# Performance work log

Measured on AMD Instinct MI355X. Metric: run time of the kernel, lower is better.

Reference implementation:

```python
import jax, jax.numpy as jnp
import numpy as np

B, T, D, H = 2, 2048, 1024, 16
DK = D // H
SCALE = 1.0 / float(np.sqrt(DK))


def setup_inputs() -> dict:
    key0 = jax.random.key(0)
    ks = jax.random.split(key0, 12)
    std = 0.02
    inp = {
        "query": jax.random.normal(ks[0], (B, T, D), jnp.float32),
        "key": jax.random.normal(ks[1], (B, T, D), jnp.float32),
        "value": jax.random.normal(ks[2], (B, T, D), jnp.float32),
        # weights stored torch-style: out = x @ W.T + b, W is [D, D]
        "Wq": jax.random.normal(ks[3], (D, D), jnp.float32) * std,
        "bq": jnp.zeros((D,), jnp.float32),
        "Wk": jax.random.normal(ks[4], (D, D), jnp.float32) * std,
        "bk": jnp.zeros((D,), jnp.float32),
        "Wv": jax.random.normal(ks[5], (D, D), jnp.float32) * std,
        "bv": jnp.zeros((D,), jnp.float32),
        "Wo": jax.random.normal(ks[6], (D, D), jnp.float32) * std,
        "bo": jnp.zeros((D,), jnp.float32),
        # causal mask: True = masked out (matches masked_fill semantics)
        "attn_mask": jnp.triu(jnp.ones((T, T), jnp.bool_), k=1),
        # no padding (all False) to keep every softmax row valid
        "key_padding_mask": jnp.zeros((B, T), jnp.bool_),
    }
    return inp


def reference(query, key, value, Wq, bq, Wk, bk, Wv, bv, Wo, bo,
              attn_mask, key_padding_mask):
    Bq, Tq, _ = query.shape
    Tk = key.shape[1]
    # QKV projections, split into heads: [B, T, H, DK]
    q = (query @ Wq.T + bq).reshape(Bq, Tq, H, DK)
    k = (key @ Wk.T + bk).reshape(Bq, Tk, H, DK)
    v = (value @ Wv.T + bv).reshape(Bq, Tk, H, DK)
    # scaled dot-product scores: [B, H, Tq, Tk]
    scores = jnp.einsum("bqhd,bkhd->bhqk", q, k) * jnp.float32(SCALE)
    neg_inf = jnp.float32(-jnp.inf)
    scores = jnp.where(attn_mask[None, None, :, :], neg_inf, scores)
    scores = jnp.where(key_padding_mask[:, None, None, :], neg_inf, scores)
    attn = jax.nn.softmax(scores, axis=-1)
    out = jnp.einsum("bhqk,bkhd->bqhd", attn, v).reshape(Bq, Tq, D)
    return out @ Wo.T + bo
```

## Files before the change

kernel.cpp:

```cpp
#include <hip/hip_runtime.h>
#include <hip/hip_bf16.h>
#include <stdint.h>

#define B_   2
#define T_   2048
#define D_   1024
#define H_   16
#define DK_  64
#define KL2_ 0.18033688f

typedef __attribute__((ext_vector_type(8))) short   short8;
typedef __attribute__((ext_vector_type(4))) float   floatx4;
typedef unsigned short ushort_t;
typedef unsigned int   uint_t;

__device__ __forceinline__ ushort_t f32_to_bf16(float f) {
    union { float f; unsigned int u; } v; v.f = f;
    unsigned int r = v.u + 0x7fffu + ((v.u >> 16) & 1u);
    return (ushort_t)(r >> 16);
}

__device__ __forceinline__ uint_t pk_bf16(float lo, float hi) {
    uint_t ulo = __builtin_bit_cast(uint_t, lo) + 0x8000u;
    uint_t uhi = __builtin_bit_cast(uint_t, hi) + 0x8000u;
    return __builtin_amdgcn_perm(uhi, ulo, 0x07060302);
}

__device__ __forceinline__ void async_copy16(const ushort_t* g, ushort_t* l) {
    typedef const unsigned int __attribute__((address_space(1)))* gp_t;
    typedef       unsigned int __attribute__((address_space(3)))* lp_t;
    __builtin_amdgcn_global_load_lds((gp_t)(uintptr_t)g, (lp_t)(uintptr_t)l, 16, 0, 0);
}

__global__ __launch_bounds__(256) void cast_all_kernel(
    const float* __restrict__ q, const float* __restrict__ k, const float* __restrict__ v,
    const float* __restrict__ wq, const float* __restrict__ wk,
    const float* __restrict__ wv, const float* __restrict__ wo,
    ushort_t* __restrict__ oq, ushort_t* __restrict__ ok, ushort_t* __restrict__ ov,
    ushort_t* __restrict__ owq, ushort_t* __restrict__ owk,
    ushort_t* __restrict__ owv, ushort_t* __restrict__ owo)
{
    const int NTD4 = (B_ * T_ * D_) / 4;
    const int NW4  = (D_ * D_) / 4;
    int i = blockIdx.x * 256 + threadIdx.x;
    const float* s; ushort_t* d; int off;
    if (i < NTD4)              { s = q; d = oq; off = i; }
    else if (i < 2 * NTD4)     { s = k; d = ok; off = i - NTD4; }
    else if (i < 3 * NTD4)     { s = v; d = ov; off = i - 2 * NTD4; }
    else {
        int w = i - 3 * NTD4;
        int seg = w / NW4;  off = w - seg * NW4;
        s = (seg == 0) ? wq : (seg == 1) ? wk : (seg == 2) ? wv : wo;
        d = (seg == 0) ? owq : (seg == 1) ? owk : (seg == 2) ? owv : owo;
    }
    float4 x = ((const float4*)s)[off];
    ushort4 o;
    o.x = f32_to_bf16(x.x); o.y = f32_to_bf16(x.y);
    o.z = f32_to_bf16(x.z); o.w = f32_to_bf16(x.w);
    ((ushort4*)d)[off] = o;
}

#define BM 128
#define BK 32

template<int MODE, int NI>
__device__ __forceinline__ void gemm_bt_device(
    const ushort_t* __restrict__ A, const ushort_t* __restrict__ W,
    const float* __restrict__ bias, void* __restrict__ outp,
    int m0, int n0, ushort_t* sm, float oscale)
{
    const int tid  = threadIdx.x;
    const int lane = tid & 63;
    const int wv   = tid >> 6;
    const int wm   = (wv >> 1) * 64;
    const int wn   = (wv & 1) * (NI * 16);
    const int cl   = lane & 15;
    const int qd   = lane >> 4;
    const int sw4  = (cl >> 1) & 3;

    floatx4 acc[4][NI];
    const floatx4 z4 = {0.f, 0.f, 0.f, 0.f};
    #pragma unroll
    for (int mi = 0; mi < 4; ++mi)
        #pragma unroll
        for (int ni = 0; ni < NI; ++ni) acc[mi][ni] = z4;

    const int r0 = tid >> 2;
    const int cg = (tid & 3) ^ ((r0 >> 1) & 3);
    const ushort_t* Ag0 = A + (size_t)(m0 + r0) * 1024 + cg * 8;
    const ushort_t* Ag1 = A + (size_t)(m0 + 64 + r0) * 1024 + cg * 8;
    const ushort_t* Wg0 = W + (size_t)(n0 + r0) * 1024 + cg * 8;
    const ushort_t* Wg1 = W + (size_t)(n0 + 64 + r0) * 1024 + cg * 8;
    ushort_t* As0 = sm + tid * 8;
    ushort_t* As1 = sm + 2048 + tid * 8;
    ushort_t* Bs0 = sm + 4096 + tid * 8;
    ushort_t* Bs1 = sm + 6144 + tid * 8;

    for (int k0 = 0; k0 < 1024; k0 += BK) {
        async_copy16(Ag0 + k0, As0);
        async_copy16(Ag1 + k0, As1);
        async_copy16(Wg0 + k0, Bs0);
        if (NI == 4) async_copy16(Wg1 + k0, Bs1);
        __syncthreads();

        short8 af[4], bfr[NI];
        #pragma unroll
        for (int mi = 0; mi < 4; ++mi)
            af[mi] = *(const short8*)(sm + (wm + mi * 16 + cl) * 32 + (qd ^ sw4) * 8);
        #pragma unroll
        for (int ni = 0; ni < NI; ++ni)
            bfr[ni] = *(const short8*)(sm + 4096 + (wn + ni * 16 + cl) * 32 + (qd ^ sw4) * 8);

        #pragma unroll
        for (int mi = 0; mi < 4; ++mi)
            #pragma unroll
            for (int ni = 0; ni < NI; ++ni)
                acc[mi][ni] = __builtin_amdgcn_mfma_f32_16x16x32_bf16(
                    af[mi], bfr[ni], acc[mi][ni], 0, 0, 0);
        __syncthreads();
    }

    #pragma unroll
    for (int mi = 0; mi < 4; ++mi) {
        #pragma unroll
        for (int ni = 0; ni < NI; ++ni) {
            const int n = n0 + wn + ni * 16 + cl;
            const float bn = bias[n];
            if (MODE == 0) {
                float* out = (float*)outp;
                #pragma unroll
                for (int r = 0; r < 4; ++r) {
                    const int m = m0 + wm + mi * 16 + qd * 4 + r;
                    out[(size_t)m * D_ + n] = acc[mi][ni][r] + bn;
                }
            } else if (MODE == 1) {
                ushort_t* out = (ushort_t*)outp;
                const int h = n >> 6, dk = n & 63;
                #pragma unroll
                for (int r = 0; r < 4; ++r) {
                    const int m = m0 + wm + mi * 16 + qd * 4 + r;
                    const int b = m >> 11, t = m & (T_ - 1);
                    out[(((size_t)(b * H_ + h)) * T_ + t) * DK_ + dk] =
                        f32_to_bf16((acc[mi][ni][r] + bn) * oscale);
                }
            } else {
                ushort_t* out = (ushort_t*)outp;
                const int h = n >> 6, dk = n & 63;
                const int mb = m0 + wm + mi * 16 + qd * 4;
                const int b = mb >> 11, t0 = mb & (T_ - 1);
                const int tsw = (t0 & ~60) | ((t0 & 48) >> 2) | ((t0 & 12) << 2);
                ushort4 o;
                o.x = f32_to_bf16(acc[mi][ni][0] + bn);
                o.y = f32_to_bf16(acc[mi][ni][1] + bn);
                o.z = f32_to_bf16(acc[mi][ni][2] + bn);
                o.w = f32_to_bf16(acc[mi][ni][3] + bn);
                *(ushort4*)(out + (((size_t)(b * H_ + h)) * DK_ + dk) * T_ + tsw) = o;
            }
        }
    }
}

__global__ __launch_bounds__(256) void gemm_qkv_kernel(
    const ushort_t* __restrict__ Xq, const ushort_t* __restrict__ Xk, const ushort_t* __restrict__ Xv,
    const ushort_t* __restrict__ Wq, const ushort_t* __restrict__ Wk, const ushort_t* __restrict__ Wv,
    const float* __restrict__ bq, const float* __restrict__ bk, const float* __restrict__ bv,
    ushort_t* __restrict__ Q, ushort_t* __restrict__ K, ushort_t* __restrict__ Vt)
{
    __shared__ __align__(16) ushort_t sm[8192];
    const int m0 = blockIdx.x * BM, n0 = blockIdx.y * 128;
    if (blockIdx.z == 0)      gemm_bt_device<1, 4>(Xq, Wq, bq, Q,  m0, n0, sm, KL2_);
    else if (blockIdx.z == 1) gemm_bt_device<1, 4>(Xk, Wk, bk, K,  m0, n0, sm, 1.0f);
    else                      gemm_bt_device<2, 4>(Xv, Wv, bv, Vt, m0, n0, sm, 1.0f);
}

__global__ __launch_bounds__(256) void gemm_o_kernel(
    const ushort_t* __restrict__ A, const ushort_t* __restrict__ W,
    const float* __restrict__ bias, float* __restrict__ out)
{
    __shared__ __align__(16) ushort_t sm[8192];
    gemm_bt_device<0, 2>(A, W, bias, out, blockIdx.x * BM, blockIdx.y * 64, sm, 1.0f);
}

__global__ __launch_bounds__(256, 2) void attn_kernel(
    const ushort_t* __restrict__ Q, const ushort_t* __restrict__ K,
    const ushort_t* __restrict__ Vs, ushort_t* __restrict__ O)
{
    __shared__ __align__(16) ushort_t sm[32768];
    const int tid  = threadIdx.x;
    const int lane = tid & 63;
    const int wv   = tid >> 6;
    const int cl   = lane & 15;
    const int qd   = lane >> 4;
    const int swz  = cl & 7;
    const int h = blockIdx.x & (H_ - 1), b = blockIdx.x >> 4;
    const int p   = blockIdx.y;
    const int btA = 31 - p;

    const ushort_t* Qh = Q  + ((size_t)(b * H_ + h) * T_) * DK_;
    const ushort_t* Kh = K  + ((size_t)(b * H_ + h) * T_) * DK_;
    const ushort_t* Vh = Vs + ((size_t)(b * H_ + h) * DK_) * T_;

    const int sr  = tid >> 3;
    const int sc  = tid & 7;
    const int scg = sc ^ (sr & 7);

    auto stage_step = [&](int s) {
        const int kbase = ((s <= btA) ? s : (s - btA - 1)) << 6;
        ushort_t* Kb = sm + (s & 3) * 8192;
        ushort_t* Vb = Kb + 4096;
        #pragma unroll
        for (int rr = 0; rr < 2; ++rr) {
            const int r = rr * 32 + sr;
            async_copy16(Kh + (size_t)(kbase + r) * DK_ + scg * 8, Kb + r * 64 + sc * 8);
            async_copy16(Vh + (size_t)r * T_ + kbase + scg * 8,    Vb + r * 64 + sc * 8);
        }
    };

    int qw = btA * 64 + wv * 16;
    short8 qf0 = *(const short8*)(Qh + (size_t)(qw + cl) * DK_ + qd * 8);
    short8 qf1 = *(const short8*)(Qh + (size_t)(qw + cl) * DK_ + 32 + qd * 8);

    stage_step(0);
    stage_step(1);

    const floatx4 z4 = {0.f, 0.f, 0.f, 0.f};
    floatx4 oaccT[4] = {z4, z4, z4, z4};
    float l_ = 0.f;

    auto flush = [&](int q0w) {
        float l = l_;
        l += __shfl_xor(l, 16, 64);
        l += __shfl_xor(l, 32, 64);
        const float inv = 1.0f / l;
        ushort_t* Ob = O + ((size_t)(b * T_ + q0w + cl)) * D_ + h * DK_ + qd * 4;
        #pragma unroll
        for (int dt = 0; dt < 4; ++dt) {
            ushort4 o;
            o.x = f32_to_bf16(oaccT[dt][0] * inv);
            o.y = f32_to_bf16(oaccT[dt][1] * inv);
            o.z = f32_to_bf16(oaccT[dt][2] * inv);
            o.w = f32_to_bf16(oaccT[dt][3] * inv);
            *(ushort4*)(Ob + dt * 16) = o;
        }
    };

    auto compute_step = [&](int s) {
        const bool inA  = (s <= btA);
        const int kbase = (inA ? s : (s - btA - 1)) << 6;
        const bool diag = inA ? (s == btA) : (s == 32);
        ushort_t* cb = sm + (s & 3) * 8192;
        short8 kb[4][2];
        #pragma unroll
        for (int m = 0; m < 4; ++m)
            #pragma unroll
            for (int i = 0; i < 2; ++i)
                kb[m][i] = *(const short8*)(cb + (m * 16 + cl) * 64 + ((i * 4 + qd) ^ swz) * 8);
        floatx4 sacc[4] = {z4, z4, z4, z4};
        #pragma unroll
        for (int i = 0; i < 2; ++i)
            #pragma unroll
            for (int m = 0; m < 4; ++m)
                sacc[m] = __builtin_amdgcn_mfma_f32_16x16x32_bf16(
                    kb[m][i], (i ? qf1 : qf0), sacc[m], 0, 0, 0);
        const int qabs = qw + cl;
        float pr[4][4];
        if (diag) {
            #pragma unroll
            for (int c = 0; c < 4; ++c)
                #pragma unroll
                for (int r = 0; r < 4; ++r) {
                    const bool keep = (kbase + c * 16 + qd * 4 + r) <= qabs;
                    const float e = __builtin_amdgcn_exp2f(sacc[c][r]);
                    pr[c][r] = keep ? e : 0.f;
                    l_ += pr[c][r];
                }
        } else {
            #pragma unroll
            for (int c = 0; c < 4; ++c)
                #pragma unroll
                for (int r = 0; r < 4; ++r) {
                    pr[c][r] = __builtin_amdgcn_exp2f(sacc[c][r]);
                    l_ += pr[c][r];
                }
        }
        short8 va2[4][2];
        #pragma unroll
        for (int dt = 0; dt < 4; ++dt)
            #pragma unroll
            for (int h2 = 0; h2 < 2; ++h2)
                va2[dt][h2] = *(const short8*)(cb + 4096 + (dt * 16 + cl) * 64 +
                                               ((qd * 2 + h2) ^ swz) * 8);
        #pragma unroll
        for (int cp = 0; cp < 2; ++cp) {
            union { uint_t u[4]; short8 v; } pb;
            pb.u[0] = pk_bf16(pr[cp * 2][0],     pr[cp * 2][1]);
            pb.u[1] = pk_bf16(pr[cp * 2][2],     pr[cp * 2][3]);
            pb.u[2] = pk_bf16(pr[cp * 2 + 1][0], pr[cp * 2 + 1][1]);
            pb.u[3] = pk_bf16(pr[cp * 2 + 1][2], pr[cp * 2 + 1][3]);
            #pragma unroll
            for (int dt = 0; dt < 4; ++dt)
                oaccT[dt] = __builtin_amdgcn_mfma_f32_16x16x32_bf16(
                    va2[dt][cp], pb.v, oaccT[dt], 0, 0, 0);
        }
        if (s == btA) {
            flush(qw);
            #pragma unroll
            for (int dt = 0; dt < 4; ++dt) oaccT[dt] = z4;
            l_ = 0.f;
            qw = p * 64 + wv * 16;
            qf0 = *(const short8*)(Qh + (size_t)(qw + cl) * DK_ + qd * 8);
            qf1 = *(const short8*)(Qh + (size_t)(qw + cl) * DK_ + 32 + qd * 8);
        }
    };

    for (int g = 0; g < 17; ++g) {
        const int s0 = g * 2;
        __syncthreads();
        if (s0 + 2 <= 32) stage_step(s0 + 2);
        if (s0 + 3 <= 32) stage_step(s0 + 3);
        compute_step(s0);
        if (s0 + 1 <= 32) compute_step(s0 + 1);
    }
    flush(qw);
}

extern "C" void kernel_launch(void* const* d_in, const int* in_sizes, int n_in,
                              void* d_out, int out_size, void* d_ws, size_t ws_size,
                              hipStream_t stream)
{
    const float* q_in = (const float*)d_in[0];
    const float* k_in = (const float*)d_in[1];
    const float* v_in = (const float*)d_in[2];
    const float* Wq   = (const float*)d_in[3];
    const float* bq   = (const float*)d_in[4];
    const float* Wk   = (const float*)d_in[5];
    const float* bk   = (const float*)d_in[6];
    const float* Wv   = (const float*)d_in[7];
    const float* bv   = (const float*)d_in[8];
    const float* Wo   = (const float*)d_in[9];
    const float* bo   = (const float*)d_in[10];
    float* out = (float*)d_out;

    const size_t NTD = (size_t)B_ * T_ * D_;
    const size_t NW  = (size_t)D_ * D_;
    ushort_t* ws  = (ushort_t*)d_ws;
    ushort_t* Xq  = ws;
    ushort_t* Xk  = Xq + NTD;
    ushort_t* Xv  = Xk + NTD;
    ushort_t* Wqb = Xv + NTD;
    ushort_t* Wkb = Wqb + NW;
    ushort_t* Wvb = Wkb + NW;
    ushort_t* Wob = Wvb + NW;
    ushort_t* Qd  = Wob + NW;
    ushort_t* Kd  = Qd + NTD;
    ushort_t* Vtd = Kd + NTD;
    ushort_t* Od  = Vtd + NTD;

    const int total4 = (int)((3 * NTD + 4 * NW) / 4);
    cast_all_kernel<<<dim3(total4 / 256), dim3(256), 0, stream>>>(
        q_in, k_in, v_in, Wq, Wk, Wv, Wo,
        Xq, Xk, Xv, Wqb, Wkb, Wvb, Wob);

    gemm_qkv_kernel<<<dim3(32, 8, 3), dim3(256), 0, stream>>>(
        Xq, Xk, Xv, Wqb, Wkb, Wvb, bq, bk, bv, Qd, Kd, Vtd);

    attn_kernel<<<dim3(32, 16), dim3(256), 0, stream>>>(Qd, Kd, Vtd, Od);

    gemm_o_kernel<<<dim3(32, 16), dim3(256), 0, stream>>>(Od, Wob, bo, out);
}
```

Baseline: 213.8 us.

## Replace QKV GEMM with 256x256-tile 8-wave double-buffered async-copy kernel

Swaps the 128-wide QKV projection GEMM for a new kernel using 256x256 output tiles, 512 threads (8 waves) and 128 KB of dynamic LDS. Global-to-LDS async copies are double-buffered and interleaved with MFMA quadrants under s_setprio and barriers. A block-index remap groups tiles to improve L2 reuse. The aim is higher arithmetic intensity and better overlap of loads with MFMA work, at the cost of very high LDS use, low occupancy and many barriers.

```diff
diff --git a/kernel.cpp b/kernel.cpp
--- a/kernel.cpp
+++ b/kernel.cpp
@@ -160,25 +160,230 @@
     }
 }
 
-__global__ __launch_bounds__(256) void gemm_qkv_kernel(
-    const ushort_t* __restrict__ Xq, const ushort_t* __restrict__ Xk, const ushort_t* __restrict__ Xv,
-    const ushort_t* __restrict__ Wq, const ushort_t* __restrict__ Wk, const ushort_t* __restrict__ Wv,
-    const float* __restrict__ bq, const float* __restrict__ bk, const float* __restrict__ bv,
-    ushort_t* __restrict__ Q, ushort_t* __restrict__ K, ushort_t* __restrict__ Vt)
-{
-    __shared__ __align__(16) ushort_t sm[8192];
-    const int m0 = blockIdx.x * BM, n0 = blockIdx.y * 128;
-    if (blockIdx.z == 0)      gemm_bt_device<1, 4>(Xq, Wq, bq, Q,  m0, n0, sm, KL2_);
-    else if (blockIdx.z == 1) gemm_bt_device<1, 4>(Xk, Wk, bk, K,  m0, n0, sm, 1.0f);
-    else                      gemm_bt_device<2, 4>(Xv, Wv, bv, Vt, m0, n0, sm, 1.0f);
-}
-
 __global__ __launch_bounds__(256) void gemm_o_kernel(
     const ushort_t* __restrict__ A, const ushort_t* __restrict__ W,
     const float* __restrict__ bias, float* __restrict__ out)
 {
     __shared__ __align__(16) ushort_t sm[8192];
     gemm_bt_device<0, 2>(A, W, bias, out, blockIdx.x * BM, blockIdx.y * 64, sm, 1.0f);
+}
+
+
+__device__ __forceinline__ void ldA4(short8 (&af)[4][2], const ushort_t* base, int coff) {
+    #pragma unroll
+    for (int mi = 0; mi < 4; ++mi) {
+        af[mi][0] = *(const short8*)(base + mi * 1024 + coff);
+        af[mi][1] = *(const short8*)(base + mi * 1024 + (coff ^ 32));
+    }
+}
+__device__ __forceinline__ void ldB2(short8 (&bf)[2][2], const ushort_t* base, int coff) {
+    #pragma unroll
+    for (int ni = 0; ni < 2; ++ni) {
+        bf[ni][0] = *(const short8*)(base + ni * 1024 + coff);
+        bf[ni][1] = *(const short8*)(base + ni * 1024 + (coff ^ 32));
+    }
+}
+
+template<int MQ, int NQ>
+__device__ __forceinline__ void quad16(floatx4 (&acc)[8][4],
+                                       const short8 (&af)[4][2],
+                                       const short8 (&bf)[2][2])
+{
+    __builtin_amdgcn_s_setprio(1);
+    #pragma unroll
+    for (int mi = 0; mi < 4; ++mi)
+        #pragma unroll
+        for (int ni = 0; ni < 2; ++ni) {
+            acc[MQ * 4 + mi][NQ * 2 + ni] = __builtin_amdgcn_mfma_f32_16x16x32_bf16(
+                af[mi][0], bf[ni][0], acc[MQ * 4 + mi][NQ * 2 + ni], 0, 0, 0);
+            acc[MQ * 4 + mi][NQ * 2 + ni] = __builtin_amdgcn_mfma_f32_16x16x32_bf16(
+                af[mi][1], bf[ni][1], acc[MQ * 4 + mi][NQ * 2 + ni], 0, 0, 0);
+        }
+    __builtin_amdgcn_s_setprio(0);
+}
+
+__global__ void __launch_bounds__(512, 2) gemm_qkv8_kernel(
+    const ushort_t* __restrict__ Xq, const ushort_t* __restrict__ Xk, const ushort_t* __restrict__ Xv,
+    const ushort_t* __restrict__ Wqw, const ushort_t* __restrict__ Wkw, const ushort_t* __restrict__ Wvw,
+    const float* __restrict__ bq, const float* __restrict__ bk, const float* __restrict__ bv,
+    ushort_t* __restrict__ Qo, ushort_t* __restrict__ Ko, ushort_t* __restrict__ Vto)
+{
+    extern __shared__ __align__(16) ushort_t sm[];
+
+    const int bid    = blockIdx.x;
+    const int gid    = (bid & 7) * 24 + (bid >> 3);
+    const int m_tile = gid / 12;
+    const int n_tile = gid - m_tile * 12;
+    const int m0     = m_tile * 256;
+    const int seg    = n_tile >> 2;
+    const int n0     = (n_tile & 3) * 256;
+
+    const ushort_t* A    = (seg == 0) ? Xq  : (seg == 1) ? Xk  : Xv;
+    const ushort_t* W    = (seg == 0) ? Wqw : (seg == 1) ? Wkw : Wvw;
+    const float*    bias = (seg == 0) ? bq  : (seg == 1) ? bk  : bv;
+
+    const int tid  = threadIdx.x;
+    const int lane = tid & 63;
+    const int wv   = tid >> 6;
+    const int wm   = wv >> 2;
+    const int wn   = wv & 3;
+    const int cl   = lane & 15;
+    const int qd   = lane >> 4;
+    const int swz  = cl & 7;
+    const int coff = (qd ^ swz) * 8;
+
+    const int r0 = tid >> 3;
+    const int c0 = (tid & 7) ^ (r0 & 7);
+    const ushort_t* gA = A + (size_t)(m0 + r0) * 1024 + c0 * 8;
+    const ushort_t* gB = W + (size_t)(n0 + r0) * 1024 + c0 * 8;
+    ushort_t* lbase = sm + tid * 8;
+
+    auto stage = [&](int t, int op, int h) {
+        if (t >= 16) return;
+        const ushort_t* g = (op ? gB : gA) + (size_t)h * 131072 + (size_t)t * 64;
+        ushort_t* l = lbase + (size_t)((t & 1) * 4 + op * 2 + h) * 8192;
+        async_copy16(g, l);
+        async_copy16(g + 65536, l + 4096);
+    };
+
+    const ushort_t* A0 = sm + (0 * 4 + 0 * 2 + wm) * 8192 + cl * 64;
+    const ushort_t* A1 = A0 + 4 * 8192;
+    const ushort_t* B0 = sm + (0 * 4 + 1 * 2 + (wn >> 1)) * 8192 + (wn & 1) * 4096 + cl * 64;
+    const ushort_t* B1 = B0 + 4 * 8192;
+
+    floatx4 acc[8][4];
+    const floatx4 z4 = {0.f, 0.f, 0.f, 0.f};
+    #pragma unroll
+    for (int i = 0; i < 8; ++i)
+        #pragma unroll
+        for (int j = 0; j < 4; ++j) acc[i][j] = z4;
+
+    stage(0, 0, 0); stage(0, 0, 1); stage(0, 1, 0); stage(0, 1, 1);
+    stage(1, 1, 0); stage(1, 1, 1);
+    asm volatile("s_waitcnt vmcnt(4)" ::: "memory");
+    __builtin_amdgcn_s_barrier();
+
+    short8 af[4][2], bf0[2][2], bf1[2][2];
+
+    #pragma unroll 1
+    for (int it = 0; it < 7; ++it) {
+        const int u = 2 * it, v = u + 1;
+        ldA4(af, A0, coff); ldB2(bf0, B0, coff);
+        stage(v, 0, 0);
+        __builtin_amdgcn_s_barrier();
+        quad16<0, 0>(acc, af, bf0);
+        __builtin_amdgcn_s_barrier();
+        ldB2(bf1, B0 + 2048, coff);
+        stage(v, 0, 1);
+        __builtin_amdgcn_s_barrier();
+        quad16<0, 1>(acc, af, bf1);
+        __builtin_amdgcn_s_barrier();
+        ldA4(af, A0 + 4096, coff);
+        stage(u + 2, 1, 0);
+        __builtin_amdgcn_s_barrier();
+        quad16<1, 1>(acc, af, bf1);
+        __builtin_amdgcn_s_barrier();
+        stage(u + 2, 1, 1);
+        asm volatile("s_waitcnt vmcnt(4)" ::: "memory");
+        __builtin_amdgcn_s_barrier();
+        quad16<1, 0>(acc, af, bf0);
+        __builtin_amdgcn_s_barrier();
+        ldA4(af, A1, coff); ldB2(bf0, B1, coff);
+        stage(u + 2, 0, 0);
+        __builtin_amdgcn_s_barrier();
+        quad16<0, 0>(acc, af, bf0);
+        __builtin_amdgcn_s_barrier();
+        ldB2(bf1, B1 + 2048, coff);
+        stage(u + 2, 0, 1);
+        __builtin_amdgcn_s_barrier();
+        quad16<0, 1>(acc, af, bf1);
+        __builtin_amdgcn_s_barrier();
+        ldA4(af, A1 + 4096, coff);
+        stage(v + 2, 1, 0);
+        __builtin_amdgcn_s_barrier();
+        quad16<1, 1>(acc, af, bf1);
+        __builtin_amdgcn_s_barrier();
+        stage(v + 2, 1, 1);
+        asm volatile("s_waitcnt vmcnt(4)" ::: "memory");
+        __builtin_amdgcn_s_barrier();
+        quad16<1, 0>(acc, af, bf0);
+        __builtin_amdgcn_s_barrier();
+    }
+
+    ldA4(af, A0, coff); ldB2(bf0, B0, coff);
+    stage(15, 0, 0);
+    __builtin_amdgcn_s_barrier();
+    quad16<0, 0>(acc, af, bf0);
+    __builtin_amdgcn_s_barrier();
+    ldB2(bf1, B0 + 2048, coff);
+    stage(15, 0, 1);
+    __builtin_amdgcn_s_barrier();
+    quad16<0, 1>(acc, af, bf1);
+    __builtin_amdgcn_s_barrier();
+    ldA4(af, A0 + 4096, coff);
+    __builtin_amdgcn_s_barrier();
+    quad16<1, 1>(acc, af, bf1);
+    __builtin_amdgcn_s_barrier();
+    asm volatile("s_waitcnt vmcnt(0)" ::: "memory");
+    __builtin_amdgcn_s_barrier();
+    quad16<1, 0>(acc, af, bf0);
+    __builtin_amdgcn_s_barrier();
+    ldA4(af, A1, coff); ldB2(bf0, B1, coff);
+    __builtin_amdgcn_s_barrier();
+    quad16<0, 0>(acc, af, bf0);
+    __builtin_amdgcn_s_barrier();
+    ldB2(bf1, B1 + 2048, coff);
+    __builtin_amdgcn_s_barrier();
+    quad16<0, 1>(acc, af, bf1);
+    __builtin_amdgcn_s_barrier();
+    ldA4(af, A1 + 4096, coff);
+    __builtin_amdgcn_s_barrier();
+    quad16<1, 1>(acc, af, bf1);
+    __builtin_amdgcn_s_barrier();
+    quad16<1, 0>(acc, af, bf0);
+
+    float bn[4];
+    #pragma unroll
+    for (int nf = 0; nf < 4; ++nf)
+        bn[nf] = bias[n0 + wn * 64 + nf * 16 + cl];
+
+    if (seg < 2) {
+        ushort_t* out = (seg == 0) ? Qo : Ko;
+        const float oscale = (seg == 0) ? KL2_ : 1.0f;
+        #pragma unroll
+        for (int mf = 0; mf < 8; ++mf) {
+            #pragma unroll
+            for (int nf = 0; nf < 4; ++nf) {
+                const int n = n0 + wn * 64 + nf * 16 + cl;
+                const int h = n >> 6, dk = n & 63;
+                #pragma unroll
+                for (int r = 0; r < 4; ++r) {
+                    const int m = m0 + wm * 128 + mf * 16 + qd * 4 + r;
+                    const int b = m >> 11, t = m & (T_ - 1);
+                    out[(((size_t)(b * H_ + h)) * T_ + t) * DK_ + dk] =
+                        f32_to_bf16((acc[mf][nf][r] + bn[nf]) * oscale);
+                }
+            }
+        }
+    } else {
+        #pragma unroll
+        for (int mf = 0; mf < 8; ++mf) {
+            #pragma unroll
+            for (int nf = 0; nf < 4; ++nf) {
+                const int n = n0 + wn * 64 + nf * 16 + cl;
+                const int h = n >> 6, dk = n & 63;
+                const int mb = m0 + wm * 128 + mf * 16 + qd * 4;
+                const int b = mb >> 11, t0 = mb & (T_ - 1);
+                const int tsw = (t0 & ~60) | ((t0 & 48) >> 2) | ((t0 & 12) << 2);
+                ushort4 o;
+                o.x = f32_to_bf16(acc[mf][nf][0] + bn[nf]);
+                o.y = f32_to_bf16(acc[mf][nf][1] + bn[nf]);
+                o.z = f32_to_bf16(acc[mf][nf][2] + bn[nf]);
+                o.w = f32_to_bf16(acc[mf][nf][3] + bn[nf]);
+                *(ushort4*)(Vto + (((size_t)(b * H_ + h)) * DK_ + dk) * T_ + tsw) = o;
+            }
+        }
+    }
 }
 
 __global__ __launch_bounds__(256, 2) void attn_kernel(
@@ -361,7 +566,13 @@
         q_in, k_in, v_in, Wq, Wk, Wv, Wo,
         Xq, Xk, Xv, Wqb, Wkb, Wvb, Wob);
 
-    gemm_qkv_kernel<<<dim3(32, 8, 3), dim3(256), 0, stream>>>(
+    static bool s_attr = false;
+    if (!s_attr) {
+        (void)hipFuncSetAttribute((const void*)gemm_qkv8_kernel,
+                                  hipFuncAttributeMaxDynamicSharedMemorySize, 131072);
+        s_attr = true;
+    }
+    gemm_qkv8_kernel<<<dim3(192), dim3(512), 131072, stream>>>(
         Xq, Xk, Xv, Wqb, Wkb, Wvb, bq, bk, bv, Qd, Kd, Vtd);
 
     attn_kernel<<<dim3(32, 16), dim3(256), 0, stream>>>(Qd, Kd, Vtd, Od);
```

Result: no change. 211.6 us (-1.0%).
